# Kernel tuning notes

Measured on AMD Instinct MI355X. Metric: run time of the kernel, lower is better.

Reference implementation:

```python
import jax, jax.numpy as jnp
import numpy as np

ENC_DIM = 256
DEC_DIM = 256
INT_DIM = 256


def setup_inputs() -> dict:
    key = jax.random.key(0)
    k1, k2, k3, k4, k5 = jax.random.split(key, 5)
    B, T = 64, 2048
    encoder_states = jax.random.normal(k1, (B, T, ENC_DIM), dtype=jnp.float32)
    decoder_state = jax.random.normal(k2, (B, DEC_DIM), dtype=jnp.float32)
    s1 = 1.0 / np.sqrt(ENC_DIM)
    s2 = 1.0 / np.sqrt(DEC_DIM)
    s3 = 1.0 / np.sqrt(INT_DIM)
    w1 = jax.random.uniform(k3, (INT_DIM, ENC_DIM), jnp.float32, -s1, s1)
    w2 = jax.random.uniform(k4, (INT_DIM, DEC_DIM), jnp.float32, -s2, s2)
    v = jax.random.uniform(k5, (1, INT_DIM), jnp.float32, -s3, s3)
    return {"encoder_states": encoder_states, "decoder_state": decoder_state,
            "w1": w1, "w2": w2, "v": v}


def reference(encoder_states, decoder_state, w1, w2, v):
    # scores: v @ tanh(W1 e_t + W2 d) for all t at once
    enc_proj = jnp.einsum('bte,ie->bti', encoder_states, w1)      # [B,T,I]
    dec_proj = jnp.einsum('bd,id->bi', decoder_state, w2)          # [B,I]
    scores = jnp.einsum('bti,oi->bt', jnp.tanh(enc_proj + dec_proj[:, None, :]), v)  # [B,T]
    attention_probs = jax.nn.softmax(scores, axis=1)[:, :, None]   # [B,T,1]
    final_context_vec = jnp.sum(attention_probs * encoder_states, axis=1)  # [B,E]
    return final_context_vec, attention_probs
```

## Files before the change

kernel.cpp:

```cpp
#include <hip/hip_runtime.h>
#include <hip/hip_bf16.h>
#include <math.h>

#define Bq 64
#define Tq 2048
#define Eq 256
#define Dq 256
#define Iq 256

using short8  = __attribute__((ext_vector_type(8))) short;
using floatx4 = __attribute__((ext_vector_type(4))) float;

__device__ __forceinline__ float fast_tanh(float x) {
    float e = __expf(2.0f * x);
    return 1.0f - 2.0f / (e + 1.0f);
}

__device__ __forceinline__ ushort f2bf(float x) {
    union { __hip_bfloat16 h; ushort u; } c;
    c.h = __float2bfloat16(x);
    return c.u;
}

__global__ __launch_bounds__(256) void w1_cvt_kernel(
    const float* __restrict__ w1, ushort* __restrict__ w1b)
{
    const int idx = (blockIdx.x * 256 + threadIdx.x) * 4;
    float4 f = *(const float4*)&w1[idx];
    ushort4 u;
    u.x = f2bf(f.x); u.y = f2bf(f.y); u.z = f2bf(f.z); u.w = f2bf(f.w);
    *(ushort4*)&w1b[idx] = u;
}

__global__ __launch_bounds__(256) void dec_proj_kernel(
    const float* __restrict__ dec, const float* __restrict__ w2,
    float* __restrict__ dproj)
{
    const int b = blockIdx.x;
    const int i = threadIdx.x;
    __shared__ float dls[Dq];
    dls[i] = dec[b * Dq + i];
    __syncthreads();
    const float* w2r = w2 + i * Dq;
    float acc = 0.f;
    #pragma unroll 8
    for (int d = 0; d < Dq; ++d) acc += dls[d] * w2r[d];
    dproj[b * Iq + i] = acc;
}

__global__ __launch_bounds__(256) void scores_mfma_kernel(
    const float*  __restrict__ enc,
    const ushort* __restrict__ w1b,
    const float*  __restrict__ v,
    const float*  __restrict__ dproj,
    float* __restrict__ scores)
{
    const int b   = blockIdx.y;
    const int t0  = blockIdx.x * 64;
    const int tid = threadIdx.x;
    const int w   = tid >> 6;
    const int l   = tid & 63;
    const int l15 = l & 15;
    const int lq  = l >> 4;

    __shared__ ushort As[64 * 72];
    __shared__ ushort Bs[256 * 72];
    __shared__ float  vls[Iq], dls[Iq];
    __shared__ float  red[64][5];

    vls[tid] = v[tid];
    dls[tid] = dproj[b * Iq + tid];

    floatx4 acc[4][4];
    #pragma unroll
    for (int mi = 0; mi < 4; ++mi)
        #pragma unroll
        for (int ni = 0; ni < 4; ++ni)
            acc[mi][ni] = (floatx4)0.f;

    const float* encB = enc + ((size_t)b * Tq + t0) * Eq;

    for (int k0 = 0; k0 < Eq; k0 += 64) {
        #pragma unroll
        for (int r = 0; r < 4; ++r) {
            const int idx = tid + 256 * r;
            const int row = idx >> 4;
            const int c4  = (idx & 15) * 4;
            float4 f = *(const float4*)&encB[row * Eq + k0 + c4];
            ushort4 u;
            u.x = f2bf(f.x); u.y = f2bf(f.y); u.z = f2bf(f.z); u.w = f2bf(f.w);
            *(ushort4*)&As[row * 72 + c4] = u;
        }
        #pragma unroll
        for (int r = 0; r < 8; ++r) {
            const int idx = tid + 256 * r;
            const int row = idx >> 3;
            const int c8  = (idx & 7) * 8;
            short8 u = *(const short8*)&w1b[row * Eq + k0 + c8];
            *(short8*)&Bs[row * 72 + c8] = u;
        }
        __syncthreads();
        #pragma unroll
        for (int ks = 0; ks < 2; ++ks) {
            const int kloc = ks * 32 + lq * 8;
            short8 af[4], bf[4];
            #pragma unroll
            for (int mi = 0; mi < 4; ++mi)
                af[mi] = *(const short8*)&As[(mi * 16 + l15) * 72 + kloc];
            #pragma unroll
            for (int ni = 0; ni < 4; ++ni)
                bf[ni] = *(const short8*)&Bs[(w * 64 + ni * 16 + l15) * 72 + kloc];
            #pragma unroll
            for (int mi = 0; mi < 4; ++mi)
                #pragma unroll
                for (int ni = 0; ni < 4; ++ni)
                    acc[mi][ni] = __builtin_amdgcn_mfma_f32_16x16x32_bf16(
                        af[mi], bf[ni], acc[mi][ni], 0, 0, 0);
        }
        __syncthreads();
    }

    float part[4][4];
    #pragma unroll
    for (int mi = 0; mi < 4; ++mi)
        #pragma unroll
        for (int r = 0; r < 4; ++r) part[mi][r] = 0.f;

    #pragma unroll
    for (int ni = 0; ni < 4; ++ni) {
        const int i  = w * 64 + ni * 16 + l15;
        const float vi = vls[i];
        const float dp = dls[i];
        #pragma unroll
        for (int mi = 0; mi < 4; ++mi)
            #pragma unroll
            for (int r = 0; r < 4; ++r)
                part[mi][r] += vi * fast_tanh(acc[mi][ni][r] + dp);
    }
    #pragma unroll
    for (int mi = 0; mi < 4; ++mi)
        #pragma unroll
        for (int r = 0; r < 4; ++r) {
            float s = part[mi][r];
            s += __shfl_xor(s, 1);
            s += __shfl_xor(s, 2);
            s += __shfl_xor(s, 4);
            s += __shfl_xor(s, 8);
            if (l15 == 0) red[mi * 16 + lq * 4 + r][w] = s;
        }
    __syncthreads();
    if (tid < 64) {
        const float s = red[tid][0] + red[tid][1] + red[tid][2] + red[tid][3];
        scores[(size_t)b * Tq + t0 + tid] = s;
    }
}

__global__ __launch_bounds__(256) void softmax_kernel(float* __restrict__ probs)
{
    const int b = blockIdx.x;
    float* row = probs + (size_t)b * Tq;
    const int tid = threadIdx.x;
    __shared__ float sred[256];

    float vals[8];
    float lmax = -INFINITY;
    #pragma unroll
    for (int j = 0; j < 8; ++j) {
        vals[j] = row[tid + 256 * j];
        lmax = fmaxf(lmax, vals[j]);
    }
    sred[tid] = lmax;
    __syncthreads();
    for (int s = 128; s > 0; s >>= 1) {
        if (tid < s) sred[tid] = fmaxf(sred[tid], sred[tid + s]);
        __syncthreads();
    }
    const float m = sred[0];
    __syncthreads();

    float lsum = 0.f;
    #pragma unroll
    for (int j = 0; j < 8; ++j) {
        vals[j] = __expf(vals[j] - m);
        lsum += vals[j];
    }
    sred[tid] = lsum;
    __syncthreads();
    for (int s = 128; s > 0; s >>= 1) {
        if (tid < s) sred[tid] += sred[tid + s];
        __syncthreads();
    }
    const float inv = 1.0f / sred[0];
    #pragma unroll
    for (int j = 0; j < 8; ++j) row[tid + 256 * j] = vals[j] * inv;
}

__global__ __launch_bounds__(256) void context_kernel(
    const float* __restrict__ enc, const float* __restrict__ probs,
    float* __restrict__ ctx)
{
    const int b  = blockIdx.y;
    const int t0 = blockIdx.x * 256;
    const int e  = threadIdx.x;
    __shared__ float p[256];
    p[threadIdx.x] = probs[(size_t)b * Tq + t0 + threadIdx.x];
    __syncthreads();
    const float* encP = enc + ((size_t)b * Tq + t0) * Eq + e;
    float a = 0.f;
    #pragma unroll 8
    for (int t = 0; t < 256; ++t) a += p[t] * encP[t * Eq];
    atomicAdd(&ctx[b * Eq + e], a);
}

extern "C" void kernel_launch(void* const* d_in, const int* in_sizes, int n_in,
                              void* d_out, int out_size, void* d_ws, size_t ws_size,
                              hipStream_t stream) {
    const float* enc = (const float*)d_in[0];
    const float* dec = (const float*)d_in[1];
    const float* w1  = (const float*)d_in[2];
    const float* w2  = (const float*)d_in[3];
    const float* v   = (const float*)d_in[4];

    float* out   = (float*)d_out;
    float* ctx   = out;
    float* probs = out + Bq * Eq;

    float*  dproj = (float*)d_ws;
    ushort* w1b   = (ushort*)((char*)d_ws + Bq * Iq * sizeof(float));

    hipMemsetAsync(ctx, 0, Bq * Eq * sizeof(float), stream);

    w1_cvt_kernel<<<dim3((Iq * Eq) / 1024), dim3(256), 0, stream>>>(w1, w1b);
    dec_proj_kernel<<<dim3(Bq), dim3(256), 0, stream>>>(dec, w2, dproj);
    scores_mfma_kernel<<<dim3(Tq / 64, Bq), dim3(256), 0, stream>>>(enc, w1b, v, dproj, probs);
    softmax_kernel<<<dim3(Bq), dim3(256), 0, stream>>>(probs);
    context_kernel<<<dim3(Tq / 256, Bq), dim3(256), 0, stream>>>(enc, probs, ctx);
}
```

Measured before the change: 251.3 us.

## Fuse softmax into scores and context kernels, async-load pre-swizzled W1

Removes the separate softmax kernel. The scores kernel now writes exp(score) and atomically adds the per-batch denominator, and the context kernel normalizes the probabilities on the fly. It skips max subtraction, which relies on scores staying small enough not to overflow exp. W1 is pre-converted into a k-chunked layout and streamed into LDS with global_load_lds, the two prep kernels are merged into one launch, and the context kernel uses float4 loads with an in-block reduction before the atomics. The intent is to cut launches, a global round trip and W1 staging overhead.

```diff
diff --git a/kernel.cpp b/kernel.cpp
--- a/kernel.cpp
+++ b/kernel.cpp
@@ -22,38 +22,47 @@
     return c.u;
 }
 
-__global__ __launch_bounds__(256) void w1_cvt_kernel(
-    const float* __restrict__ w1, ushort* __restrict__ w1b)
-{
-    const int idx = (blockIdx.x * 256 + threadIdx.x) * 4;
-    float4 f = *(const float4*)&w1[idx];
-    ushort4 u;
-    u.x = f2bf(f.x); u.y = f2bf(f.y); u.z = f2bf(f.z); u.w = f2bf(f.w);
-    *(ushort4*)&w1b[idx] = u;
-}
-
-__global__ __launch_bounds__(256) void dec_proj_kernel(
+__device__ __forceinline__ void async_load16(const void* g, void* l) {
+    __builtin_amdgcn_global_load_lds(
+        (const __attribute__((address_space(1))) void*)g,
+        (__attribute__((address_space(3))) void*)l, 16, 0, 0);
+}
+
+__global__ __launch_bounds__(256) void prep_kernel(
+    const float* __restrict__ w1, ushort* __restrict__ w1sw,
     const float* __restrict__ dec, const float* __restrict__ w2,
     float* __restrict__ dproj)
 {
-    const int b = blockIdx.x;
-    const int i = threadIdx.x;
-    __shared__ float dls[Dq];
-    dls[i] = dec[b * Dq + i];
-    __syncthreads();
-    const float* w2r = w2 + i * Dq;
-    float acc = 0.f;
-    #pragma unroll 8
-    for (int d = 0; d < Dq; ++d) acc += dls[d] * w2r[d];
-    dproj[b * Iq + i] = acc;
+    if (blockIdx.x < 32) {
+        const int kc = blockIdx.x;
+        const int i  = threadIdx.x;
+        const float* src = w1 + i * Eq + kc * 8;
+        float4 f0 = *(const float4*)src;
+        float4 f1 = *(const float4*)(src + 4);
+        ushort u[8] = { f2bf(f0.x), f2bf(f0.y), f2bf(f0.z), f2bf(f0.w),
+                        f2bf(f1.x), f2bf(f1.y), f2bf(f1.z), f2bf(f1.w) };
+        *(short8*)&w1sw[(kc * 256 + i) * 8] = *(short8*)u;
+    } else {
+        const int b = blockIdx.x - 32;
+        const int i = threadIdx.x;
+        __shared__ float dls[Dq];
+        dls[i] = dec[b * Dq + i];
+        __syncthreads();
+        const float* w2r = w2 + i * Dq;
+        float acc = 0.f;
+        #pragma unroll 8
+        for (int d = 0; d < Dq; ++d) acc += dls[d] * w2r[d];
+        dproj[b * Iq + i] = acc;
+    }
 }
 
 __global__ __launch_bounds__(256) void scores_mfma_kernel(
     const float*  __restrict__ enc,
-    const ushort* __restrict__ w1b,
+    const ushort* __restrict__ w1sw,
     const float*  __restrict__ v,
     const float*  __restrict__ dproj,
-    float* __restrict__ scores)
+    float* __restrict__ escore,
+    float* __restrict__ denom)
 {
     const int b   = blockIdx.y;
     const int t0  = blockIdx.x * 64;
@@ -64,9 +73,8 @@
     const int lq  = l >> 4;
 
     __shared__ ushort As[64 * 72];
-    __shared__ ushort Bs[256 * 72];
+    __shared__ ushort Bs[16384];
     __shared__ float  vls[Iq], dls[Iq];
-    __shared__ float  red[64][5];
 
     vls[tid] = v[tid];
     dls[tid] = dproj[b * Iq + tid];
@@ -81,6 +89,12 @@
     const float* encB = enc + ((size_t)b * Tq + t0) * Eq;
 
     for (int k0 = 0; k0 < Eq; k0 += 64) {
+        const ushort* gb = w1sw + (size_t)(k0 >> 3) * 256 * 8;
+        #pragma unroll
+        for (int r = 0; r < 8; ++r) {
+            const int qbase = r * 256 + w * 64;
+            async_load16(gb + (qbase + l) * 8, Bs + qbase * 8);
+        }
         #pragma unroll
         for (int r = 0; r < 4; ++r) {
             const int idx = tid + 256 * r;
@@ -91,31 +105,23 @@
             u.x = f2bf(f.x); u.y = f2bf(f.y); u.z = f2bf(f.z); u.w = f2bf(f.w);
             *(ushort4*)&As[row * 72 + c4] = u;
         }
-        #pragma unroll
-        for (int r = 0; r < 8; ++r) {
-            const int idx = tid + 256 * r;
-            const int row = idx >> 3;
-            const int c8  = (idx & 7) * 8;
-            short8 u = *(const short8*)&w1b[row * Eq + k0 + c8];
-            *(short8*)&Bs[row * 72 + c8] = u;
-        }
         __syncthreads();
         #pragma unroll
         for (int ks = 0; ks < 2; ++ks) {
             const int kloc = ks * 32 + lq * 8;
-            short8 af[4], bf[4];
+            short8 af[4], bfv[4];
             #pragma unroll
             for (int mi = 0; mi < 4; ++mi)
                 af[mi] = *(const short8*)&As[(mi * 16 + l15) * 72 + kloc];
             #pragma unroll
             for (int ni = 0; ni < 4; ++ni)
-                bf[ni] = *(const short8*)&Bs[(w * 64 + ni * 16 + l15) * 72 + kloc];
+                bfv[ni] = *(const short8*)&Bs[((ks * 4 + lq) * 256 + w * 64 + ni * 16 + l15) * 8];
             #pragma unroll
             for (int mi = 0; mi < 4; ++mi)
                 #pragma unroll
                 for (int ni = 0; ni < 4; ++ni)
                     acc[mi][ni] = __builtin_amdgcn_mfma_f32_16x16x32_bf16(
-                        af[mi], bf[ni], acc[mi][ni], 0, 0, 0);
+                        af[mi], bfv[ni], acc[mi][ni], 0, 0, 0);
         }
         __syncthreads();
     }
@@ -128,7 +134,7 @@
 
     #pragma unroll
     for (int ni = 0; ni < 4; ++ni) {
-        const int i  = w * 64 + ni * 16 + l15;
+        const int i   = w * 64 + ni * 16 + l15;
         const float vi = vls[i];
         const float dp = dls[i];
         #pragma unroll
@@ -137,79 +143,79 @@
             for (int r = 0; r < 4; ++r)
                 part[mi][r] += vi * fast_tanh(acc[mi][ni][r] + dp);
     }
+
+    float* red2 = (float*)Bs;
     #pragma unroll
     for (int mi = 0; mi < 4; ++mi)
         #pragma unroll
-        for (int r = 0; r < 4; ++r) {
-            float s = part[mi][r];
-            s += __shfl_xor(s, 1);
-            s += __shfl_xor(s, 2);
-            s += __shfl_xor(s, 4);
-            s += __shfl_xor(s, 8);
-            if (l15 == 0) red[mi * 16 + lq * 4 + r][w] = s;
-        }
+        for (int r = 0; r < 4; ++r)
+            red2[(w * 64 + mi * 16 + lq * 4 + r) * 20 + l15] = part[mi][r];
     __syncthreads();
+
     if (tid < 64) {
-        const float s = red[tid][0] + red[tid][1] + red[tid][2] + red[tid][3];
-        scores[(size_t)b * Tq + t0 + tid] = s;
-    }
-}
-
-__global__ __launch_bounds__(256) void softmax_kernel(float* __restrict__ probs)
+        float s = 0.f;
+        #pragma unroll
+        for (int ww = 0; ww < 4; ++ww) {
+            const float* rp = red2 + (ww * 64 + tid) * 20;
+            float4 q0 = *(const float4*)(rp + 0);
+            float4 q1 = *(const float4*)(rp + 4);
+            float4 q2 = *(const float4*)(rp + 8);
+            float4 q3 = *(const float4*)(rp + 12);
+            s += (q0.x + q0.y + q0.z + q0.w) + (q1.x + q1.y + q1.z + q1.w)
+               + (q2.x + q2.y + q2.z + q2.w) + (q3.x + q3.y + q3.z + q3.w);
+        }
+        const float es = __expf(s);
+        escore[(size_t)b * Tq + t0 + tid] = es;
+        float tot = es;
+        tot += __shfl_xor(tot, 1);  tot += __shfl_xor(tot, 2);
+        tot += __shfl_xor(tot, 4);  tot += __shfl_xor(tot, 8);
+        tot += __shfl_xor(tot, 16); tot += __shfl_xor(tot, 32);
+        if (tid == 0) atomicAdd(&denom[b], tot);
+    }
+}
+
+__global__ __launch_bounds__(256) void context_kernel(
+    const float* __restrict__ enc, const float* __restrict__ escore,
+    const float* __restrict__ denom,
+    float* __restrict__ probs, float* __restrict__ ctx)
 {
-    const int b = blockIdx.x;
-    float* row = probs + (size_t)b * Tq;
+    const int b   = blockIdx.y;
+    const int t0  = blockIdx.x * 256;
     const int tid = threadIdx.x;
-    __shared__ float sred[256];
-
-    float vals[8];
-    float lmax = -INFINITY;
-    #pragma unroll
-    for (int j = 0; j < 8; ++j) {
-        vals[j] = row[tid + 256 * j];
-        lmax = fmaxf(lmax, vals[j]);
-    }
-    sred[tid] = lmax;
+    const int tg  = tid >> 6;
+    const int e4  = (tid & 63) * 4;
+
+    __shared__ float pv[256];
+    __shared__ float red[4][256];
+
+    const float inv = 1.0f / denom[b];
+    const float p = escore[(size_t)b * Tq + t0 + tid] * inv;
+    pv[tid] = p;
+    probs[(size_t)b * Tq + t0 + tid] = p;
     __syncthreads();
-    for (int s = 128; s > 0; s >>= 1) {
-        if (tid < s) sred[tid] = fmaxf(sred[tid], sred[tid + s]);
-        __syncthreads();
-    }
-    const float m = sred[0];
+
+    const float* encB = enc + ((size_t)b * Tq + t0) * Eq;
+    float4 a = {0.f, 0.f, 0.f, 0.f};
+    #pragma unroll 4
+    for (int tt = 0; tt < 64; ++tt) {
+        const int t = tt * 4 + tg;
+        const float pt = pv[t];
+        float4 ev = *(const float4*)&encB[t * Eq + e4];
+        a.x += pt * ev.x; a.y += pt * ev.y; a.z += pt * ev.z; a.w += pt * ev.w;
+    }
+    *(float4*)&red[tg][e4] = a;
     __syncthreads();
-
-    float lsum = 0.f;
-    #pragma unroll
-    for (int j = 0; j < 8; ++j) {
-        vals[j] = __expf(vals[j] - m);
-        lsum += vals[j];
-    }
-    sred[tid] = lsum;
-    __syncthreads();
-    for (int s = 128; s > 0; s >>= 1) {
-        if (tid < s) sred[tid] += sred[tid + s];
-        __syncthreads();
-    }
-    const float inv = 1.0f / sred[0];
-    #pragma unroll
-    for (int j = 0; j < 8; ++j) row[tid + 256 * j] = vals[j] * inv;
-}
-
-__global__ __launch_bounds__(256) void context_kernel(
-    const float* __restrict__ enc, const float* __restrict__ probs,
-    float* __restrict__ ctx)
-{
-    const int b  = blockIdx.y;
-    const int t0 = blockIdx.x * 256;
-    const int e  = threadIdx.x;
-    __shared__ float p[256];
-    p[threadIdx.x] = probs[(size_t)b * Tq + t0 + threadIdx.x];
-    __syncthreads();
-    const float* encP = enc + ((size_t)b * Tq + t0) * Eq + e;
-    float a = 0.f;
-    #pragma unroll 8
-    for (int t = 0; t < 256; ++t) a += p[t] * encP[t * Eq];
-    atomicAdd(&ctx[b * Eq + e], a);
+    if (tg == 0) {
+        float4 a0 = *(const float4*)&red[0][e4];
+        float4 a1 = *(const float4*)&red[1][e4];
+        float4 a2 = *(const float4*)&red[2][e4];
+        float4 a3 = *(const float4*)&red[3][e4];
+        float* c = ctx + b * Eq + e4;
+        atomicAdd(c + 0, a0.x + a1.x + a2.x + a3.x);
+        atomicAdd(c + 1, a0.y + a1.y + a2.y + a3.y);
+        atomicAdd(c + 2, a0.z + a1.z + a2.z + a3.z);
+        atomicAdd(c + 3, a0.w + a1.w + a2.w + a3.w);
+    }
 }
 
 extern "C" void kernel_launch(void* const* d_in, const int* in_sizes, int n_in,
@@ -225,14 +231,17 @@
     float* ctx   = out;
     float* probs = out + Bq * Eq;
 
-    float*  dproj = (float*)d_ws;
-    ushort* w1b   = (ushort*)((char*)d_ws + Bq * Iq * sizeof(float));
+    char* ws = (char*)d_ws;
+    float*  dproj = (float*)ws;
+    ushort* w1sw  = (ushort*)(ws + 262144);
+    float*  denom = (float*)(ws + 262144 + 131072);
 
     hipMemsetAsync(ctx, 0, Bq * Eq * sizeof(float), stream);
-
-    w1_cvt_kernel<<<dim3((Iq * Eq) / 1024), dim3(256), 0, stream>>>(w1, w1b);
-    dec_proj_kernel<<<dim3(Bq), dim3(256), 0, stream>>>(dec, w2, dproj);
-    scores_mfma_kernel<<<dim3(Tq / 64, Bq), dim3(256), 0, stream>>>(enc, w1b, v, dproj, probs);
-    softmax_kernel<<<dim3(Bq), dim3(256), 0, stream>>>(probs);
-    context_kernel<<<dim3(Tq / 256, Bq), dim3(256), 0, stream>>>(enc, probs, ctx);
-}
+    hipMemsetAsync(denom, 0, Bq * sizeof(float), stream);
+
+    prep_kernel<<<dim3(96), dim3(256), 0, stream>>>(w1, w1sw, dec, w2, dproj);
+    scores_mfma_kernel<<<dim3(Tq / 64, Bq), dim3(256), 0, stream>>>(
+        enc, w1sw, v, dproj, probs, denom);
+    context_kernel<<<dim3(Tq / 256, Bq), dim3(256), 0, stream>>>(
+        enc, probs, denom, probs, ctx);
+}
```

Measured after the change: 254.2 us. About the same (+1.2%).
